# Performance work log

Measured on AMD Instinct MI355X. Metric: run time of the kernel, lower is better.

## Reference

```python
import jax, jax.numpy as jnp
import numpy as np

EMBED = 768
HIDDEN = 768
HEADS = 12
HEAD_DIM = HIDDEN // HEADS


def setup_inputs() -> dict:
    key = jax.random.key(0)
    ks = jax.random.split(key, 9)
    B, S = 16, 512
    lim = 1.0 / np.sqrt(EMBED)
    def lin(kw, kb):
        W = jax.random.uniform(kw, (EMBED, HIDDEN), jnp.float32, -lim, lim)
        b = jax.random.uniform(kb, (HIDDEN,), jnp.float32, -lim, lim)
        return W, b
    Wq, bq = lin(ks[0], ks[1])
    Wk, bk = lin(ks[2], ks[3])
    Wv, bv = lin(ks[4], ks[5])
    inp = jax.random.normal(ks[6], (B, S, EMBED), jnp.float32)
    mask = jax.random.randint(ks[7], (B, S), 0, 2).astype(jnp.float32)
    return {"input": inp, "input_mask": mask,
            "Wq": Wq, "bq": bq, "Wk": Wk, "bk": bk, "Wv": Wv, "bv": bv}


def reference(input, input_mask, Wq, bq, Wk, bk, Wv, bv):
    B, S, _ = input.shape
    # projections -> (B, H, S, D)
    def proj(W, b):
        x = jnp.einsum('bse,eh->bsh', input, W) + b
        return x.reshape(B, S, HEADS, HEAD_DIM).transpose(0, 2, 1, 3)
    Q = proj(Wq, bq)
    K = proj(Wk, bk)
    V = proj(Wv, bv)
    # scores (B, H, S, S), additive mask over keys
    scores = jnp.einsum('bhqd,bhkd->bhqk', Q, K) / jnp.sqrt(jnp.float32(HEAD_DIM))
    bias = (input_mask * -1e9)[:, None, None, :]  # (B,1,1,S) broadcast over heads & queries
    weight = jax.nn.softmax(scores + bias, axis=-1)
    out = jnp.einsum('bhqk,bhkd->bhqd', weight, V)
    return out.transpose(0, 2, 1, 3).reshape(B, S, HIDDEN)
```

## Files before the change

### kernel.cpp

```cpp
#include <hip/hip_runtime.h>
#include <cstdint>
#include <cstddef>

#define B_  16
#define S_  512
#define E_  768
#define NH_ 12
#define D_  64
#define M_  (B_*S_)

typedef unsigned short u16;
typedef __attribute__((ext_vector_type(4))) float f32x4;
typedef __attribute__((ext_vector_type(8))) short bf16x8;

#define LOG2E 1.4426950408889634f

__device__ __forceinline__ u16 f2bf(float f){
  union { float fv; uint32_t u; } v; v.fv = f;
  uint32_t u = v.u;
  uint32_t r = u + 0x7fffu + ((u >> 16) & 1u);
  return (u16)(r >> 16);
}

__global__ __launch_bounds__(256) void cast_x_kernel(const float* __restrict__ x,
                                                     u16* __restrict__ xb, int n4){
  int i = blockIdx.x * 256 + threadIdx.x;
  if (i < n4){
    float4 v = reinterpret_cast<const float4*>(x)[i];
    ushort4 o;
    o.x = f2bf(v.x); o.y = f2bf(v.y); o.z = f2bf(v.z); o.w = f2bf(v.w);
    reinterpret_cast<ushort4*>(xb)[i] = o;
  }
}

__global__ __launch_bounds__(256) void transpose_w_kernel(const float* __restrict__ Wq,
                                                          const float* __restrict__ Wk,
                                                          const float* __restrict__ Wv,
                                                          u16* __restrict__ WtBase){
  __shared__ float t[32][33];
  const float* W = (blockIdx.z == 0) ? Wq : ((blockIdx.z == 1) ? Wk : Wv);
  u16* Wt = WtBase + (size_t)blockIdx.z * E_ * E_;
  int bx = blockIdx.x * 32, by = blockIdx.y * 32;
  int tx = threadIdx.x & 31, ty = threadIdx.x >> 5;
  #pragma unroll
  for (int i = 0; i < 32; i += 8)
    t[ty + i][tx] = W[(size_t)(by + ty + i) * E_ + bx + tx];
  __syncthreads();
  #pragma unroll
  for (int i = 0; i < 32; i += 8)
    Wt[(size_t)(bx + ty + i) * E_ + by + tx] = f2bf(t[tx][ty + i]);
}

__global__ __launch_bounds__(256) void qkv_gemm_kernel(
    const u16* __restrict__ Xb, const u16* __restrict__ WtBase,
    const float* __restrict__ bq, const float* __restrict__ bk, const float* __restrict__ bv,
    u16* __restrict__ Qb, u16* __restrict__ Kb, u16* __restrict__ VtB)
{
  __shared__ u16 lA[8 * 512];
  __shared__ u16 lB[8 * 512];
  const int z = blockIdx.z;
  const u16* Wt = WtBase + (size_t)z * E_ * E_;
  const float* bias = (z == 0) ? bq : ((z == 1) ? bk : bv);
  const int m0 = blockIdx.x * 128;
  const int n0 = blockIdx.y * 128;
  const int tid = threadIdx.x;
  const int lane = tid & 63;
  const int wave = tid >> 6;
  const int wm = wave & 1, wn = wave >> 1;
  const int ls = lane & 15;
  const int lk = lane >> 4;
  const int col0 = lane & 15, quad = lane >> 4;

  f32x4 acc[4][4];
  #pragma unroll
  for (int i = 0; i < 4; ++i)
    #pragma unroll
    for (int j = 0; j < 4; ++j)
      acc[i][j] = (f32x4){0.f, 0.f, 0.f, 0.f};

  #pragma unroll 1
  for (int k0 = 0; k0 < E_; k0 += 32){
    __syncthreads();
    uint4 va[2], vb[2];
    #pragma unroll
    for (int cc = 0; cc < 2; ++cc){
      int c = wave * 2 + cc;
      va[cc] = *reinterpret_cast<const uint4*>(Xb + (size_t)(m0 + c*16 + ls) * E_ + k0 + lk*8);
      vb[cc] = *reinterpret_cast<const uint4*>(Wt + (size_t)(n0 + c*16 + ls) * E_ + k0 + lk*8);
    }
    #pragma unroll
    for (int cc = 0; cc < 2; ++cc){
      int c = wave * 2 + cc;
      *reinterpret_cast<uint4*>(&lA[c*512 + lane*8]) = va[cc];
      *reinterpret_cast<uint4*>(&lB[c*512 + lane*8]) = vb[cc];
    }
    __syncthreads();
    bf16x8 af[4], bfr[4];
    #pragma unroll
    for (int mi = 0; mi < 4; ++mi)
      af[mi] = *reinterpret_cast<const bf16x8*>(&lA[(wm*4 + mi)*512 + lane*8]);
    #pragma unroll
    for (int ni = 0; ni < 4; ++ni)
      bfr[ni] = *reinterpret_cast<const bf16x8*>(&lB[(wn*4 + ni)*512 + lane*8]);
    #pragma unroll
    for (int mi = 0; mi < 4; ++mi)
      #pragma unroll
      for (int ni = 0; ni < 4; ++ni)
        acc[mi][ni] = __builtin_amdgcn_mfma_f32_16x16x32_bf16(af[mi], bfr[ni], acc[mi][ni], 0, 0, 0);
  }

  #pragma unroll
  for (int mi = 0; mi < 4; ++mi){
    #pragma unroll
    for (int ni = 0; ni < 4; ++ni){
      int n = n0 + wn*64 + ni*16 + col0;
      float bval = bias[n];
      int h = n >> 6, d = n & 63;
      #pragma unroll
      for (int r = 0; r < 4; ++r){
        int m = m0 + wm*64 + mi*16 + quad*4 + r;
        int b = m >> 9, s = m & 511;
        u16 obf = f2bf(acc[mi][ni][r] + bval);
        size_t bh = (size_t)b * NH_ + h;
        if (z == 0)      Qb[(bh * S_ + s) * D_ + d] = obf;
        else if (z == 1) Kb[(bh * S_ + s) * D_ + d] = obf;
        else             VtB[(bh * D_ + d) * S_ + s] = obf;
      }
    }
  }
}

__global__ __launch_bounds__(256) void attn_kernel(
    const u16* __restrict__ Qb, const u16* __restrict__ Kb, const u16* __restrict__ VtB,
    const float* __restrict__ mask, float* __restrict__ out)
{
  __shared__ u16 lK[2][8 * 512];
  __shared__ u16 lV[2][8 * 512];
  __shared__ u16 lP[8 * 1024];
  __shared__ float biasS[S_];
  const int bh = blockIdx.x;
  const int qt = blockIdx.y;
  const int b = bh / NH_, h = bh % NH_;
  const int tid = threadIdx.x, lane = tid & 63, wave = tid >> 6;
  const int col0 = lane & 15, quad = lane >> 4;
  const int ls = lane & 15, lk = lane >> 4;

  for (int i = tid; i < S_; i += 256)
    biasS[i] = mask[b * S_ + i] * -1e9f;

  const u16* Kbh = Kb  + (size_t)bh * S_ * D_;
  const u16* Vbh = VtB + (size_t)bh * D_ * S_;

  bf16x8 qf[2][2];
  #pragma unroll
  for (int g = 0; g < 2; ++g){
    int qrow = qt*128 + wave*32 + g*16 + col0;
    #pragma unroll
    for (int ks = 0; ks < 2; ++ks)
      qf[g][ks] = *reinterpret_cast<const bf16x8*>(
          Qb + ((size_t)bh * S_ + qrow) * D_ + ks*32 + quad*8);
  }

  uint4 rg[4];
  auto issue = [&](int st){
    if (wave < 2){
      #pragma unroll
      for (int gg = 0; gg < 4; ++gg){
        int c = wave*4 + gg, ks = c >> 2, nt = c & 3;
        rg[gg] = *reinterpret_cast<const uint4*>(
            Kbh + (size_t)(st*64 + nt*16 + ls) * D_ + ks*32 + lk*8);
      }
    } else {
      #pragma unroll
      for (int gg = 0; gg < 4; ++gg){
        int c = (wave - 2)*4 + gg, ks2 = c >> 2, nd = c & 3;
        rg[gg] = *reinterpret_cast<const uint4*>(
            Vbh + (size_t)(nd*16 + ls) * S_ + st*64 + ks2*32 + lk*8);
      }
    }
  };
  issue(0);

  f32x4 o[2][4];
  #pragma unroll
  for (int g = 0; g < 2; ++g)
    #pragma unroll
    for (int i = 0; i < 4; ++i) o[g][i] = (f32x4){0.f, 0.f, 0.f, 0.f};
  float mold[2] = {-3.0e38f, -3.0e38f};
  float lold[2] = {0.f, 0.f};

  #pragma unroll 1
  for (int st = 0; st < 8; ++st){
    const int cur = st & 1;
    if (wave < 2){
      #pragma unroll
      for (int gg = 0; gg < 4; ++gg)
        *reinterpret_cast<uint4*>(&lK[cur][(wave*4 + gg)*512 + lane*8]) = rg[gg];
    } else {
      #pragma unroll
      for (int gg = 0; gg < 4; ++gg)
        *reinterpret_cast<uint4*>(&lV[cur][((wave - 2)*4 + gg)*512 + lane*8]) = rg[gg];
    }
    __syncthreads();
    if (st < 7) issue(st + 1);

    f32x4 sc[2][4];
    #pragma unroll
    for (int g = 0; g < 2; ++g)
      #pragma unroll
      for (int nt = 0; nt < 4; ++nt) sc[g][nt] = (f32x4){0.f, 0.f, 0.f, 0.f};
    #pragma unroll
    for (int ks = 0; ks < 2; ++ks){
      bf16x8 kf[4];
      #pragma unroll
      for (int nt = 0; nt < 4; ++nt)
        kf[nt] = *reinterpret_cast<const bf16x8*>(&lK[cur][(ks*4 + nt)*512 + lane*8]);
      #pragma unroll
      for (int g = 0; g < 2; ++g)
        #pragma unroll
        for (int nt = 0; nt < 4; ++nt)
          sc[g][nt] = __builtin_amdgcn_mfma_f32_16x16x32_bf16(kf[nt], qf[g][ks], sc[g][nt], 0, 0, 0);
    }

    float4 bb[4];
    #pragma unroll
    for (int nt = 0; nt < 4; ++nt)
      bb[nt] = *reinterpret_cast<const float4*>(&biasS[st*64 + nt*16 + quad*4]);

    #pragma unroll
    for (int g = 0; g < 2; ++g){
      float vv[4][4];
      #pragma unroll
      for (int nt = 0; nt < 4; ++nt){
        vv[nt][0] = sc[g][nt][0] * 0.125f + bb[nt].x;
        vv[nt][1] = sc[g][nt][1] * 0.125f + bb[nt].y;
        vv[nt][2] = sc[g][nt][2] * 0.125f + bb[nt].z;
        vv[nt][3] = sc[g][nt][3] * 0.125f + bb[nt].w;
      }
      float mrow = vv[0][0];
      #pragma unroll
      for (int nt = 0; nt < 4; ++nt)
        #pragma unroll
        for (int r = 0; r < 4; ++r)
          mrow = fmaxf(mrow, vv[nt][r]);
      mrow = fmaxf(mrow, __shfl_xor(mrow, 16, 64));
      mrow = fmaxf(mrow, __shfl_xor(mrow, 32, 64));
      float mnew = fmaxf(mold[g], mrow);
      float alpha = exp2f((mold[g] - mnew) * LOG2E);
      float rsum = 0.f;
      #pragma unroll
      for (int nt = 0; nt < 4; ++nt){
        ushort4 pw;
        float p0 = exp2f((vv[nt][0] - mnew) * LOG2E);
        float p1 = exp2f((vv[nt][1] - mnew) * LOG2E);
        float p2 = exp2f((vv[nt][2] - mnew) * LOG2E);
        float p3 = exp2f((vv[nt][3] - mnew) * LOG2E);
        rsum += (p0 + p1) + (p2 + p3);
        pw.x = f2bf(p0); pw.y = f2bf(p1); pw.z = f2bf(p2); pw.w = f2bf(p3);
        int addr = (wave*2 + g)*1024 + (nt >> 1)*512
                 + (((nt & 1)*2 + (quad >> 1))*16 + col0)*8 + (quad & 1)*4;
        *reinterpret_cast<ushort4*>(&lP[addr]) = pw;
      }
      rsum += __shfl_xor(rsum, 16, 64);
      rsum += __shfl_xor(rsum, 32, 64);
      lold[g] = alpha * lold[g] + rsum;
      mold[g] = mnew;
      #pragma unroll
      for (int r = 0; r < 4; ++r){
        float ar = __shfl(alpha, (lane & 48) | (quad*4 + r), 64);
        #pragma unroll
        for (int nd = 0; nd < 4; ++nd)
          o[g][nd][r] *= ar;
      }
    }

    #pragma unroll
    for (int ks2 = 0; ks2 < 2; ++ks2){
      bf16x8 pf0 = *reinterpret_cast<const bf16x8*>(&lP[(wave*2 + 0)*1024 + ks2*512 + lane*8]);
      bf16x8 pf1 = *reinterpret_cast<const bf16x8*>(&lP[(wave*2 + 1)*1024 + ks2*512 + lane*8]);
      #pragma unroll
      for (int nd = 0; nd < 4; ++nd){
        bf16x8 vf = *reinterpret_cast<const bf16x8*>(&lV[cur][(ks2*4 + nd)*512 + lane*8]);
        o[0][nd] = __builtin_amdgcn_mfma_f32_16x16x32_bf16(pf0, vf, o[0][nd], 0, 0, 0);
        o[1][nd] = __builtin_amdgcn_mfma_f32_16x16x32_bf16(pf1, vf, o[1][nd], 0, 0, 0);
      }
    }
  }

  #pragma unroll
  for (int g = 0; g < 2; ++g){
    #pragma unroll
    for (int r = 0; r < 4; ++r){
      int s = qt*128 + wave*32 + g*16 + quad*4 + r;
      float lr = __shfl(lold[g], (lane & 48) | (quad*4 + r), 64);
      float inv = 1.0f / lr;
      #pragma unroll
      for (int nd = 0; nd < 4; ++nd){
        int d = nd*16 + col0;
        out[((size_t)b * S_ + s) * E_ + h*D_ + d] = o[g][nd][r] * inv;
      }
    }
  }
}

extern "C" void kernel_launch(void* const* d_in, const int* in_sizes, int n_in,
                              void* d_out, int out_size, void* d_ws, size_t ws_size,
                              hipStream_t stream){
  const float* X    = (const float*)d_in[0];
  const float* mask = (const float*)d_in[1];
  const float* Wq   = (const float*)d_in[2];
  const float* bq   = (const float*)d_in[3];
  const float* Wk   = (const float*)d_in[4];
  const float* bk   = (const float*)d_in[5];
  const float* Wv   = (const float*)d_in[6];
  const float* bv   = (const float*)d_in[7];
  float* out = (float*)d_out;

  u16* Xb = (u16*)d_ws;
  u16* Wt = Xb + (size_t)M_ * E_;
  u16* Qb = Wt + (size_t)3 * E_ * E_;
  u16* Kb = Qb + (size_t)M_ * E_;
  u16* Vt = Kb + (size_t)M_ * E_;

  cast_x_kernel<<<(M_ * E_ / 4 + 255) / 256, 256, 0, stream>>>(X, Xb, M_ * E_ / 4);
  transpose_w_kernel<<<dim3(24, 24, 3), 256, 0, stream>>>(Wq, Wk, Wv, Wt);
  qkv_gemm_kernel<<<dim3(64, 6, 3), 256, 0, stream>>>(Xb, Wt, bq, bk, bv, Qb, Kb, Vt);
  attn_kernel<<<dim3(192, 4), 256, 0, stream>>>(Qb, Kb, Vt, mask, out);
}
```

Before: 235.3 us.

## Merge prep kernels and deepen GEMM K-step with swizzled LDS layout

Merges the X cast and weight transpose into one prep kernel launch, which removes one launch and its gap. The QKV GEMM now processes 64 elements of K per iteration instead of 32, halving the number of barrier pairs. Global loads are reorganised so each lane fetches contiguous 16-byte chunks. LDS stores and reads use an XOR swizzle to avoid bank conflicts. In exchange the GEMM uses twice the LDS and more registers per block, which may lower occupancy.

Result: faster. 223.3 us (-5.1%).

```diff
diff --git a/kernel.cpp b/kernel.cpp
--- a/kernel.cpp
+++ b/kernel.cpp
@@ -22,33 +22,35 @@
   return (u16)(r >> 16);
 }
 
-__global__ __launch_bounds__(256) void cast_x_kernel(const float* __restrict__ x,
-                                                     u16* __restrict__ xb, int n4){
-  int i = blockIdx.x * 256 + threadIdx.x;
-  if (i < n4){
-    float4 v = reinterpret_cast<const float4*>(x)[i];
+__global__ __launch_bounds__(256) void prep_kernel(
+    const float* __restrict__ X, u16* __restrict__ Xb,
+    const float* __restrict__ Wq, const float* __restrict__ Wk,
+    const float* __restrict__ Wv, u16* __restrict__ WtBase)
+{
+  __shared__ float t[32][33];
+  const int bx = blockIdx.x;
+  if (bx < 6144){
+    int i = bx * 256 + threadIdx.x;
+    float4 v = reinterpret_cast<const float4*>(X)[i];
     ushort4 o;
     o.x = f2bf(v.x); o.y = f2bf(v.y); o.z = f2bf(v.z); o.w = f2bf(v.w);
-    reinterpret_cast<ushort4*>(xb)[i] = o;
-  }
-}
-
-__global__ __launch_bounds__(256) void transpose_w_kernel(const float* __restrict__ Wq,
-                                                          const float* __restrict__ Wk,
-                                                          const float* __restrict__ Wv,
-                                                          u16* __restrict__ WtBase){
-  __shared__ float t[32][33];
-  const float* W = (blockIdx.z == 0) ? Wq : ((blockIdx.z == 1) ? Wk : Wv);
-  u16* Wt = WtBase + (size_t)blockIdx.z * E_ * E_;
-  int bx = blockIdx.x * 32, by = blockIdx.y * 32;
-  int tx = threadIdx.x & 31, ty = threadIdx.x >> 5;
-  #pragma unroll
-  for (int i = 0; i < 32; i += 8)
-    t[ty + i][tx] = W[(size_t)(by + ty + i) * E_ + bx + tx];
-  __syncthreads();
-  #pragma unroll
-  for (int i = 0; i < 32; i += 8)
-    Wt[(size_t)(bx + ty + i) * E_ + by + tx] = f2bf(t[tx][ty + i]);
+    reinterpret_cast<ushort4*>(Xb)[i] = o;
+  } else {
+    int tt = bx - 6144;
+    int z = tt / 576, rem = tt % 576;
+    int byi = rem / 24, bxi = rem % 24;
+    const float* W = (z == 0) ? Wq : ((z == 1) ? Wk : Wv);
+    u16* Wt = WtBase + (size_t)z * E_ * E_;
+    int bx0 = bxi * 32, by0 = byi * 32;
+    int tx = threadIdx.x & 31, ty = threadIdx.x >> 5;
+    #pragma unroll
+    for (int i = 0; i < 32; i += 8)
+      t[ty + i][tx] = W[(size_t)(by0 + ty + i) * E_ + bx0 + tx];
+    __syncthreads();
+    #pragma unroll
+    for (int i = 0; i < 32; i += 8)
+      Wt[(size_t)(bx0 + ty + i) * E_ + by0 + tx] = f2bf(t[tx][ty + i]);
+  }
 }
 
 __global__ __launch_bounds__(256) void qkv_gemm_kernel(
@@ -56,8 +58,8 @@
     const float* __restrict__ bq, const float* __restrict__ bk, const float* __restrict__ bv,
     u16* __restrict__ Qb, u16* __restrict__ Kb, u16* __restrict__ VtB)
 {
-  __shared__ u16 lA[8 * 512];
-  __shared__ u16 lB[8 * 512];
+  __shared__ u16 lA[16 * 512];
+  __shared__ u16 lB[16 * 512];
   const int z = blockIdx.z;
   const u16* Wt = WtBase + (size_t)z * E_ * E_;
   const float* bias = (z == 0) ? bq : ((z == 1) ? bk : bv);
@@ -67,9 +69,10 @@
   const int lane = tid & 63;
   const int wave = tid >> 6;
   const int wm = wave & 1, wn = wave >> 1;
-  const int ls = lane & 15;
-  const int lk = lane >> 4;
   const int col0 = lane & 15, quad = lane >> 4;
+  const int srow = lane >> 2, soct = lane & 3;
+  const int sslot = soct*16 + (srow ^ (soct << 1));
+  const int rslot = quad*16 + (col0 ^ (quad << 1));
 
   f32x4 acc[4][4];
   #pragma unroll
@@ -79,34 +82,39 @@
       acc[i][j] = (f32x4){0.f, 0.f, 0.f, 0.f};
 
   #pragma unroll 1
-  for (int k0 = 0; k0 < E_; k0 += 32){
+  for (int k0 = 0; k0 < E_; k0 += 64){
     __syncthreads();
-    uint4 va[2], vb[2];
-    #pragma unroll
-    for (int cc = 0; cc < 2; ++cc){
-      int c = wave * 2 + cc;
-      va[cc] = *reinterpret_cast<const uint4*>(Xb + (size_t)(m0 + c*16 + ls) * E_ + k0 + lk*8);
-      vb[cc] = *reinterpret_cast<const uint4*>(Wt + (size_t)(n0 + c*16 + ls) * E_ + k0 + lk*8);
-    }
-    #pragma unroll
-    for (int cc = 0; cc < 2; ++cc){
-      int c = wave * 2 + cc;
-      *reinterpret_cast<uint4*>(&lA[c*512 + lane*8]) = va[cc];
-      *reinterpret_cast<uint4*>(&lB[c*512 + lane*8]) = vb[cc];
+    uint4 va[4], vb[4];
+    #pragma unroll
+    for (int i = 0; i < 4; ++i){
+      int rh = i >> 1, kh = i & 1;
+      int grow = rh*64 + wave*16 + srow;
+      va[i] = *reinterpret_cast<const uint4*>(Xb + (size_t)(m0 + grow) * E_ + k0 + kh*32 + soct*8);
+      vb[i] = *reinterpret_cast<const uint4*>(Wt + (size_t)(n0 + grow) * E_ + k0 + kh*32 + soct*8);
+    }
+    #pragma unroll
+    for (int i = 0; i < 4; ++i){
+      int rh = i >> 1, kh = i & 1;
+      int c = (rh*4 + wave)*2 + kh;
+      *reinterpret_cast<uint4*>(&lA[c*512 + sslot*8]) = va[i];
+      *reinterpret_cast<uint4*>(&lB[c*512 + sslot*8]) = vb[i];
     }
     __syncthreads();
-    bf16x8 af[4], bfr[4];
-    #pragma unroll
-    for (int mi = 0; mi < 4; ++mi)
-      af[mi] = *reinterpret_cast<const bf16x8*>(&lA[(wm*4 + mi)*512 + lane*8]);
-    #pragma unroll
-    for (int ni = 0; ni < 4; ++ni)
-      bfr[ni] = *reinterpret_cast<const bf16x8*>(&lB[(wn*4 + ni)*512 + lane*8]);
-    #pragma unroll
-    for (int mi = 0; mi < 4; ++mi)
+    #pragma unroll
+    for (int ks = 0; ks < 2; ++ks){
+      bf16x8 af[4], bfr[4];
+      #pragma unroll
+      for (int mi = 0; mi < 4; ++mi)
+        af[mi] = *reinterpret_cast<const bf16x8*>(&lA[((wm*4 + mi)*2 + ks)*512 + rslot*8]);
       #pragma unroll
       for (int ni = 0; ni < 4; ++ni)
-        acc[mi][ni] = __builtin_amdgcn_mfma_f32_16x16x32_bf16(af[mi], bfr[ni], acc[mi][ni], 0, 0, 0);
+        bfr[ni] = *reinterpret_cast<const bf16x8*>(&lB[((wn*4 + ni)*2 + ks)*512 + rslot*8]);
+      #pragma unroll
+      for (int mi = 0; mi < 4; ++mi)
+        #pragma unroll
+        for (int ni = 0; ni < 4; ++ni)
+          acc[mi][ni] = __builtin_amdgcn_mfma_f32_16x16x32_bf16(af[mi], bfr[ni], acc[mi][ni], 0, 0, 0);
+    }
   }
 
   #pragma unroll
@@ -322,8 +330,7 @@
   u16* Kb = Qb + (size_t)M_ * E_;
   u16* Vt = Kb + (size_t)M_ * E_;
 
-  cast_x_kernel<<<(M_ * E_ / 4 + 255) / 256, 256, 0, stream>>>(X, Xb, M_ * E_ / 4);
-  transpose_w_kernel<<<dim3(24, 24, 3), 256, 0, stream>>>(Wq, Wk, Wv, Wt);
+  prep_kernel<<<6144 + 1728, 256, 0, stream>>>(X, Xb, Wq, Wk, Wv, Wt);
   qkv_gemm_kernel<<<dim3(64, 6, 3), 256, 0, stream>>>(Xb, Wt, bq, bk, bv, Qb, Kb, Vt);
   attn_kernel<<<dim3(192, 4), 256, 0, stream>>>(Qb, Kb, Vt, mask, out);
 }
```
